# Kernel tuning notes

Hardware: AMD Instinct MI355X
Metric: run time of the kernel (lower is better)

Reference implementation:

```python
import jax, jax.numpy as jnp
import numpy as np

N_NODES = 100000
N_EDGES = 6400000
TOKEN_DIM = 16


def setup_inputs() -> dict:
    key = jax.random.key(0)
    k1, k2, k3, k4, k5 = jax.random.split(key, 5)
    x = jax.random.normal(k1, (N_NODES, 1), dtype=jnp.float32)
    edge_index = jax.random.randint(k2, (2, N_EDGES), 0, N_NODES, dtype=jnp.int64)
    # PyTorch nn.Linear init: U(-1/sqrt(fan_in), 1/sqrt(fan_in)); plain normals are fine for a correctness baseline
    w1 = jax.random.normal(k3, (TOKEN_DIM, 2), dtype=jnp.float32) * (1.0 / np.sqrt(2.0))
    b1 = jnp.zeros((TOKEN_DIM,), dtype=jnp.float32)
    w2 = jax.random.normal(k4, (TOKEN_DIM, TOKEN_DIM), dtype=jnp.float32) * (1.0 / np.sqrt(TOKEN_DIM))
    b2 = jnp.zeros((TOKEN_DIM,), dtype=jnp.float32)
    return {"x": x, "edge_index": edge_index, "w1": w1, "b1": b1, "w2": w2, "b2": b2}


def reference(x, edge_index, w1, b1, w2, b2):
    row, col = edge_index[0], edge_index[1]
    # gather-multiply: bond_e = s_row * s_col, shape [E, 1]
    bond = x[row] * x[col]
    # scatter-add into local_field, shape [N, 1]
    local_field = jax.ops.segment_sum(bond, row, num_segments=x.shape[0])
    feats = jnp.concatenate([x, local_field], axis=1)  # [N, 2]
    h = jax.nn.relu(feats @ w1.T + b1)                  # [N, token_dim]
    tokens = jax.nn.relu(h @ w2.T + b2)                 # [N, token_dim]
    return tokens
```

## Files before the change

### kernel.cpp

```cpp
#include <hip/hip_runtime.h>

#define TOKEN_DIM 16
#define RANGES 4
#define MAX_RS 25088

__global__ __launch_bounds__(1024)
void nit_phase1(const int* __restrict__ row, const int* __restrict__ col,
                const float* __restrict__ x,
                float* __restrict__ partial,
                int N, long long E, int chunkE, int RS) {
    __shared__ float acc[MAX_RS];
    const int c = blockIdx.x / RANGES;
    const int r = blockIdx.x % RANGES;
    const int base = r * RS;
    int cnt = N - base; if (cnt > RS) cnt = RS; if (cnt < 0) cnt = 0;
    const int t = threadIdx.x, nt = blockDim.x;

    for (int j = t; j < cnt; j += nt) acc[j] = 0.0f;
    __syncthreads();

    long long i0 = (long long)c * chunkE;
    long long i1 = i0 + chunkE; if (i1 > E) i1 = E;
    if (i0 < i1) {
        long long len = i1 - i0;
        long long ngrp = len >> 2;
        for (long long g = t; g < ngrp; g += nt) {
            long long idx = i0 + (g << 2);
            int4 rr = *reinterpret_cast<const int4*>(row + idx);
            int4 cc = *reinterpret_cast<const int4*>(col + idx);
            unsigned d;
            d = (unsigned)(rr.x - base); if (d < (unsigned)cnt) atomicAdd(&acc[d], x[cc.x]);
            d = (unsigned)(rr.y - base); if (d < (unsigned)cnt) atomicAdd(&acc[d], x[cc.y]);
            d = (unsigned)(rr.z - base); if (d < (unsigned)cnt) atomicAdd(&acc[d], x[cc.z]);
            d = (unsigned)(rr.w - base); if (d < (unsigned)cnt) atomicAdd(&acc[d], x[cc.w]);
        }
        for (long long idx = i0 + (ngrp << 2) + t; idx < i1; idx += nt) {
            unsigned d = (unsigned)(row[idx] - base);
            if (d < (unsigned)cnt) atomicAdd(&acc[d], x[col[idx]]);
        }
    }
    __syncthreads();

    float* dst = partial + (size_t)c * N + base;
    for (int j = t; j < cnt; j += nt) dst[j] = acc[j];
}

__global__ __launch_bounds__(256)
void nit_phase2(const float* __restrict__ x,
                const float* __restrict__ partial,
                const float* __restrict__ w1, const float* __restrict__ b1,
                const float* __restrict__ w2, const float* __restrict__ b2,
                float* __restrict__ out, int N, int C) {
    __shared__ float sw1[TOKEN_DIM * 2];
    __shared__ float sb1[TOKEN_DIM];
    __shared__ float sw2[TOKEN_DIM * TOKEN_DIM];
    __shared__ float sb2[TOKEN_DIM];
    const int t = threadIdx.x;
    if (t < TOKEN_DIM * TOKEN_DIM) sw2[t] = w2[t];
    if (t < TOKEN_DIM * 2) sw1[t] = w1[t];
    if (t < TOKEN_DIM) { sb1[t] = b1[t]; sb2[t] = b2[t]; }
    __syncthreads();

    const int n = blockIdx.x * blockDim.x + t;
    if (n >= N) return;

    float s = 0.0f;
    for (int c = 0; c < C; ++c) s += partial[(size_t)c * N + n];

    const float xv = x[n];
    const float lv = xv * s;

    float h[TOKEN_DIM];
#pragma unroll
    for (int j = 0; j < TOKEN_DIM; ++j) {
        float v = fmaf(xv, sw1[2 * j], fmaf(lv, sw1[2 * j + 1], sb1[j]));
        h[j] = v > 0.0f ? v : 0.0f;
    }

    float o[TOKEN_DIM];
#pragma unroll
    for (int j = 0; j < TOKEN_DIM; ++j) {
        float v = sb2[j];
#pragma unroll
        for (int k = 0; k < TOKEN_DIM; ++k) v = fmaf(h[k], sw2[j * TOKEN_DIM + k], v);
        o[j] = v > 0.0f ? v : 0.0f;
    }

    float4* op = reinterpret_cast<float4*>(out + (size_t)n * TOKEN_DIM);
#pragma unroll
    for (int j = 0; j < 4; ++j)
        op[j] = make_float4(o[4 * j], o[4 * j + 1], o[4 * j + 2], o[4 * j + 3]);
}

extern "C" void kernel_launch(void* const* d_in, const int* in_sizes, int n_in,
                              void* d_out, int out_size, void* d_ws, size_t ws_size,
                              hipStream_t stream) {
    const float* x  = (const float*)d_in[0];
    const int*   ei = (const int*)d_in[1];
    const float* w1 = (const float*)d_in[2];
    const float* b1 = (const float*)d_in[3];
    const float* w2 = (const float*)d_in[4];
    const float* b2 = (const float*)d_in[5];
    float* out = (float*)d_out;

    const int N = in_sizes[0];
    const long long E = in_sizes[1] / 2;
    const int* row = ei;
    const int* col = ei + E;

    int maxC = (int)(ws_size / ((size_t)N * sizeof(float)));
    int C = maxC < 1 ? 1 : (maxC > 64 ? 64 : maxC);
    const int RS = (N + RANGES - 1) / RANGES;
    long long ce = (E + C - 1) / C;
    int chunkE = (int)((ce + 3LL) & ~3LL);

    float* partial = (float*)d_ws;

    nit_phase1<<<C * RANGES, 1024, 0, stream>>>(row, col, x, partial,
                                                N, E, chunkE, RS);

    int block2 = 256;
    int grid2 = (N + block2 - 1) / block2;
    nit_phase2<<<grid2, block2, 0, stream>>>(x, partial, w1, b1, w2, b2,
                                             out, N, C);
}
```

Before: 166.5 us.

## Retune edge-chunk grid, unroll edge loads, and split partial reduction across threads

Phase 1 now uses 5 node ranges with a smaller shared-memory accumulator and up to 102 edge chunks, giving 510 blocks instead of 256. The edge loop now handles 8 edges per thread iteration through two int4 loads each for row and col. Phase 2 assigns 4 threads per node to sum the per-chunk partials and combines them through shared memory, so the larger chunk count does not lengthen the serial reduction. The cost is more partial buffers to write and read, plus 3/4 of threads idling during the MLP stage.

```diff
diff --git a/kernel.cpp b/kernel.cpp
--- a/kernel.cpp
+++ b/kernel.cpp
@@ -1,10 +1,11 @@
 #include <hip/hip_runtime.h>
 
 #define TOKEN_DIM 16
-#define RANGES 4
-#define MAX_RS 25088
+#define RANGES 5
+#define MAX_RS 20000
+#define MAX_C  102
 
-__global__ __launch_bounds__(1024)
+__global__ __launch_bounds__(1024, 8)
 void nit_phase1(const int* __restrict__ row, const int* __restrict__ col,
                 const float* __restrict__ x,
                 float* __restrict__ partial,
@@ -23,18 +24,24 @@
     long long i1 = i0 + chunkE; if (i1 > E) i1 = E;
     if (i0 < i1) {
         long long len = i1 - i0;
-        long long ngrp = len >> 2;
+        long long ngrp = len >> 3;
         for (long long g = t; g < ngrp; g += nt) {
-            long long idx = i0 + (g << 2);
-            int4 rr = *reinterpret_cast<const int4*>(row + idx);
-            int4 cc = *reinterpret_cast<const int4*>(col + idx);
+            long long idx = i0 + (g << 3);
+            int4 r0 = *reinterpret_cast<const int4*>(row + idx);
+            int4 r1 = *reinterpret_cast<const int4*>(row + idx + 4);
+            int4 c0 = *reinterpret_cast<const int4*>(col + idx);
+            int4 c1 = *reinterpret_cast<const int4*>(col + idx + 4);
             unsigned d;
-            d = (unsigned)(rr.x - base); if (d < (unsigned)cnt) atomicAdd(&acc[d], x[cc.x]);
-            d = (unsigned)(rr.y - base); if (d < (unsigned)cnt) atomicAdd(&acc[d], x[cc.y]);
-            d = (unsigned)(rr.z - base); if (d < (unsigned)cnt) atomicAdd(&acc[d], x[cc.z]);
-            d = (unsigned)(rr.w - base); if (d < (unsigned)cnt) atomicAdd(&acc[d], x[cc.w]);
+            d = (unsigned)(r0.x - base); if (d < (unsigned)cnt) atomicAdd(&acc[d], x[c0.x]);
+            d = (unsigned)(r0.y - base); if (d < (unsigned)cnt) atomicAdd(&acc[d], x[c0.y]);
+            d = (unsigned)(r0.z - base); if (d < (unsigned)cnt) atomicAdd(&acc[d], x[c0.z]);
+            d = (unsigned)(r0.w - base); if (d < (unsigned)cnt) atomicAdd(&acc[d], x[c0.w]);
+            d = (unsigned)(r1.x - base); if (d < (unsigned)cnt) atomicAdd(&acc[d], x[c1.x]);
+            d = (unsigned)(r1.y - base); if (d < (unsigned)cnt) atomicAdd(&acc[d], x[c1.y]);
+            d = (unsigned)(r1.z - base); if (d < (unsigned)cnt) atomicAdd(&acc[d], x[c1.z]);
+            d = (unsigned)(r1.w - base); if (d < (unsigned)cnt) atomicAdd(&acc[d], x[c1.w]);
         }
-        for (long long idx = i0 + (ngrp << 2) + t; idx < i1; idx += nt) {
+        for (long long idx = i0 + (ngrp << 3) + t; idx < i1; idx += nt) {
             unsigned d = (unsigned)(row[idx] - base);
             if (d < (unsigned)cnt) atomicAdd(&acc[d], x[col[idx]]);
         }
@@ -45,7 +52,7 @@
     for (int j = t; j < cnt; j += nt) dst[j] = acc[j];
 }
 
-__global__ __launch_bounds__(256)
+__global__ __launch_bounds__(256, 8)
 void nit_phase2(const float* __restrict__ x,
                 const float* __restrict__ partial,
                 const float* __restrict__ w1, const float* __restrict__ b1,
@@ -55,41 +62,55 @@
     __shared__ float sb1[TOKEN_DIM];
     __shared__ float sw2[TOKEN_DIM * TOKEN_DIM];
     __shared__ float sb2[TOKEN_DIM];
+    __shared__ float red[256];
+
     const int t = threadIdx.x;
     if (t < TOKEN_DIM * TOKEN_DIM) sw2[t] = w2[t];
     if (t < TOKEN_DIM * 2) sw1[t] = w1[t];
     if (t < TOKEN_DIM) { sb1[t] = b1[t]; sb2[t] = b2[t]; }
+
+    const int n = t & 63;
+    const int g = t >> 6;
+    const int node0 = blockIdx.x * 64;
+    const int node = node0 + n;
+
+    float s = 0.0f;
+    if (node < N) {
+        for (int c = g; c < C; c += 4) s += partial[(size_t)c * N + node];
+    }
+    red[t] = s;
     __syncthreads();
 
-    const int n = blockIdx.x * blockDim.x + t;
-    if (n >= N) return;
+    if (t < 64) {
+        const int nn = node0 + t;
+        if (nn < N) {
+            const float ssum = red[t] + red[64 + t] + red[128 + t] + red[192 + t];
+            const float xv = x[nn];
+            const float lv = xv * ssum;
 
-    float s = 0.0f;
-    for (int c = 0; c < C; ++c) s += partial[(size_t)c * N + n];
+            float h[TOKEN_DIM];
+#pragma unroll
+            for (int j = 0; j < TOKEN_DIM; ++j) {
+                float v = fmaf(xv, sw1[2 * j], fmaf(lv, sw1[2 * j + 1], sb1[j]));
+                h[j] = v > 0.0f ? v : 0.0f;
+            }
 
-    const float xv = x[n];
-    const float lv = xv * s;
+            float o[TOKEN_DIM];
+#pragma unroll
+            for (int j = 0; j < TOKEN_DIM; ++j) {
+                float v = sb2[j];
+#pragma unroll
+                for (int k = 0; k < TOKEN_DIM; ++k)
+                    v = fmaf(h[k], sw2[j * TOKEN_DIM + k], v);
+                o[j] = v > 0.0f ? v : 0.0f;
+            }
 
-    float h[TOKEN_DIM];
+            float4* op = reinterpret_cast<float4*>(out + (size_t)nn * TOKEN_DIM);
 #pragma unroll
-    for (int j = 0; j < TOKEN_DIM; ++j) {
-        float v = fmaf(xv, sw1[2 * j], fmaf(lv, sw1[2 * j + 1], sb1[j]));
-        h[j] = v > 0.0f ? v : 0.0f;
+            for (int j = 0; j < 4; ++j)
+                op[j] = make_float4(o[4 * j], o[4 * j + 1], o[4 * j + 2], o[4 * j + 3]);
+        }
     }
-
-    float o[TOKEN_DIM];
-#pragma unroll
-    for (int j = 0; j < TOKEN_DIM; ++j) {
-        float v = sb2[j];
-#pragma unroll
-        for (int k = 0; k < TOKEN_DIM; ++k) v = fmaf(h[k], sw2[j * TOKEN_DIM + k], v);
-        o[j] = v > 0.0f ? v : 0.0f;
-    }
-
-    float4* op = reinterpret_cast<float4*>(out + (size_t)n * TOKEN_DIM);
-#pragma unroll
-    for (int j = 0; j < 4; ++j)
-        op[j] = make_float4(o[4 * j], o[4 * j + 1], o[4 * j + 2], o[4 * j + 3]);
 }
 
 extern "C" void kernel_launch(void* const* d_in, const int* in_sizes, int n_in,
@@ -109,18 +130,17 @@
     const int* col = ei + E;
 
     int maxC = (int)(ws_size / ((size_t)N * sizeof(float)));
-    int C = maxC < 1 ? 1 : (maxC > 64 ? 64 : maxC);
+    int C = maxC < 1 ? 1 : (maxC > MAX_C ? MAX_C : maxC);
     const int RS = (N + RANGES - 1) / RANGES;
     long long ce = (E + C - 1) / C;
-    int chunkE = (int)((ce + 3LL) & ~3LL);
+    int chunkE = (int)((ce + 7LL) & ~7LL);
 
     float* partial = (float*)d_ws;
 
     nit_phase1<<<C * RANGES, 1024, 0, stream>>>(row, col, x, partial,
                                                 N, E, chunkE, RS);
 
-    int block2 = 256;
-    int grid2 = (N + block2 - 1) / block2;
-    nit_phase2<<<grid2, block2, 0, stream>>>(x, partial, w1, b1, w2, b2,
-                                             out, N, C);
+    int grid2 = (N + 63) / 64;
+    nit_phase2<<<grid2, 256, 0, stream>>>(x, partial, w1, b1, w2, b2,
+                                          out, N, C);
 }
```

Result: no change. 166.3 us (-0.1%).
